# Kernel tuning notes

Measured on AMD Instinct MI355X. Metric: run time of the kernel, lower is better.

Reference implementation:

```python
import jax, jax.numpy as jnp
import numpy as np

N = 12288   # nodes
E = 393216  # edges (avg degree 32)
B = 16      # graphs in batch
F_IN = 15   # node feature dim
H = 32      # hidden_dim
EMB = 64    # embedding_dim
NC = 11     # num_classes
EDIM = 2    # edge feature dim
EPS = 1e-5  # BatchNorm eps


def _bn(x, gamma, beta):
    # training-mode BatchNorm1d: biased batch variance, matches torch normalization
    mu = jnp.mean(x, axis=0)
    var = jnp.var(x, axis=0)
    return gamma * (x - mu) * jax.lax.rsqrt(var + EPS) + beta


def setup_inputs() -> dict:
    key = jax.random.key(0)
    ks = jax.random.split(key, 16)
    def p(k, shape, s=0.05):
        return jax.random.normal(k, shape, dtype=jnp.float32) * s
    z = lambda *s: jnp.zeros(s, jnp.float32)
    o = lambda *s: jnp.ones(s, jnp.float32)
    return {
        "x": jax.random.normal(ks[0], (N, F_IN), dtype=jnp.float32),
        "edge_attr": jax.random.normal(ks[1], (E, EDIM), dtype=jnp.float32),
        "w_edge": p(ks[2], (EDIM, 1)), "b_edge": z(1),
        "w1": p(ks[3], (F_IN, H)), "b1": z(H), "g1": o(H), "be1": z(H),
        "w2": p(ks[4], (H, 2 * H)), "b2": z(2 * H), "g2": o(2 * H), "be2": z(2 * H),
        "w3": p(ks[5], (2 * H, EMB)), "b3": z(EMB), "g3": o(EMB), "be3": z(EMB),
        "wf1": p(ks[6], (EMB, 512)), "bf1": z(512), "gf1": o(512), "bef1": z(512),
        "wf2": p(ks[7], (512, 256)), "bf2": z(256), "gf2": o(256), "bef2": z(256),
        "wf3": p(ks[8], (256, NC)), "bf3": z(NC),
        "edge_index": jax.random.randint(ks[9], (2, E), 0, N, dtype=jnp.int64)
                      if jax.config.jax_enable_x64 else jax.random.randint(ks[9], (2, E), 0, N),
        "batch": jnp.sort(jax.random.randint(ks[10], (N,), 0, B)),
    }


def reference(x, edge_attr, w_edge, b_edge,
              w1, b1, g1, be1, w2, b2, g2, be2, w3, b3, g3, be3,
              wf1, bf1, gf1, bef1, wf2, bf2, gf2, bef2, wf3, bf3,
              edge_index, batch):
    # edge weights: sigmoid(Linear(edge_attr)) -> [E]
    ew = jax.nn.sigmoid(edge_attr @ w_edge + b_edge)[:, 0]
    # dense adjacency with self loops, accumulate duplicates (sparse_coo.to_dense)
    loop = jnp.arange(N)
    row = jnp.concatenate([edge_index[0], loop])
    col = jnp.concatenate([edge_index[1], loop])
    w_aug = jnp.concatenate([ew, jnp.ones((N,), ew.dtype)])
    adj = jnp.zeros((N, N), ew.dtype).at[row, col].add(w_aug)
    # symmetric degree normalization D^-1/2 A D^-1/2
    deg = adj.sum(axis=1)
    dis = jnp.where(deg > 0, jax.lax.rsqrt(jnp.where(deg > 0, deg, 1.0)), 0.0)
    support = dis[:, None] * adj * dis[None, :]
    # three GCN layers: support @ x @ W + b, BN, relu
    h = jax.nn.relu(_bn(support @ x @ w1 + b1, g1, be1))
    h = jax.nn.relu(_bn(support @ h @ w2 + b2, g2, be2))
    h = jax.nn.relu(_bn(support @ h @ w3 + b3, g3, be3))
    # global max pool per graph (empty graphs -> zeros)
    seg = jax.ops.segment_max(h, batch, num_segments=B)
    cnt = jax.ops.segment_sum(jnp.ones((N,), h.dtype), batch, num_segments=B)
    emb = jnp.where(cnt[:, None] > 0, seg, 0.0)
    # MLP head (dropout = identity at inference)
    o = jax.nn.relu(_bn(emb @ wf1 + bf1, gf1, bef1))
    o = jax.nn.relu(_bn(o @ wf2 + bf2, gf2, bef2))
    logits = o @ wf3 + bf3
    return jax.nn.log_softmax(logits, axis=1), emb
```

## Files before the change

kernel.cpp:

```cpp
#include <hip/hip_runtime.h>
#include <hip/hip_bf16.h>

#define NN   12288
#define EE   393216
#define EEPAD (EE + 8*NN)
#define BG   16
#define FIN  15
#define FH1  32
#define FH2  64
#define NCL  11
#define BNEPS 1e-5f
#define NBANK 32

typedef unsigned short u16;
typedef unsigned long long u64;
static inline int cdiv(long a, long b){ return (int)((a + b - 1) / b); }

__device__ __forceinline__ int getIdx(const void* p, long i, int is64){
  return is64 ? (int)((const long long*)p)[i] : ((const int*)p)[i];
}

__global__ void k_pre(u64* deg_cnt, float* csp1, float* csp2, float* csp3,
                      const void* ei, const void* batch, int* flags){
  int g = blockIdx.x*256 + threadIdx.x;
  if (g < NN) deg_cnt[g] = 0ull;
  if (g < NBANK*128){ csp1[g] = 0.f; csp2[g] = 0.f; csp3[g] = 0.f; }
  if (blockIdx.x == 0 && threadIdx.x < 64){
    const int* a = (const int*)ei;
    unsigned long long m0 = __ballot(a[2*threadIdx.x + 1] == 0);
    const int* b = (const int*)batch;
    int j = 96*threadIdx.x;
    unsigned long long m1 = __ballot(b[2*j + 1] == 0);
    if (threadIdx.x == 0){
      flags[0] = (m0 == ~0ull) ? 1 : 0;
      flags[1] = (m1 == ~0ull) ? 1 : 0;
    }
  }
}

__global__ void k_edge(const float* ea, const float* we, const float* bedg,
                       const void* ei, const int* flags, u64* deg_cnt, int* sslot){
  int e = blockIdx.x*256 + threadIdx.x;
  if (e >= EE) return;
  int is64 = flags[0];
  float z = ea[2*e]*we[0] + ea[2*e+1]*we[1] + bedg[0];
  float w = 1.0f/(1.0f + expf(-z));
  int r = getIdx(ei, e, is64);
  u64 add = (1ull << 32) | (u64)__float2uint_rn(w * 1048576.0f);
  u64 old = atomicAdd(&deg_cnt[r], add);
  sslot[e] = (int)(old >> 32);
}

__global__ void k_scanA(const u64* deg_cnt, int* rowptr, int* bsum){
  __shared__ int sbuf[256];
  int i = blockIdx.x*256 + threadIdx.x;
  int v = ((int)(deg_cnt[i] >> 32) + 7) & ~7;
  sbuf[threadIdx.x] = v;
  __syncthreads();
  for (int off = 1; off < 256; off <<= 1){
    int add = (threadIdx.x >= off) ? sbuf[threadIdx.x - off] : 0;
    __syncthreads();
    sbuf[threadIdx.x] += add;
    __syncthreads();
  }
  rowptr[i] = sbuf[threadIdx.x] - v;
  if (threadIdx.x == 255) bsum[blockIdx.x] = sbuf[255];
}

__global__ void k_scanB(const int* bsum, const u64* deg_cnt,
                        int* rowptr, float* dis, u64* csr_p){
  __shared__ int sbx[64];
  if (threadIdx.x < 64){
    int v = (threadIdx.x < 48) ? bsum[threadIdx.x] : 0;
    sbx[threadIdx.x] = v;
  }
  __syncthreads();
  for (int off = 1; off < 64; off <<= 1){
    int add = (threadIdx.x < 64 && threadIdx.x >= off) ? sbx[threadIdx.x - off] : 0;
    __syncthreads();
    if (threadIdx.x < 64) sbx[threadIdx.x] += add;
    __syncthreads();
  }
  __syncthreads();
  int off = (blockIdx.x == 0) ? 0 : sbx[blockIdx.x - 1];
  int i = blockIdx.x*256 + threadIdx.x;
  int rp = rowptr[i] + off;
  rowptr[i] = rp;
  u64 dc = deg_cnt[i];
  float deg = 1.0f + (float)(unsigned)(dc & 0xffffffffull) * (1.0f/1048576.0f);
  dis[i] = rsqrtf(deg);
  int n = (int)(dc >> 32), np = (n + 7) & ~7;
  for (int s = rp + n; s < rp + np; s++) csr_p[s] = 0ull;
}

__global__ void k_fill(const float* ea, const float* we, const float* bedg,
                       const void* ei, const int* flags, const float* dis,
                       const int* rowptr, const int* sslot, u64* csr_p){
  int e = blockIdx.x*256 + threadIdx.x;
  if (e >= EE) return;
  int is64 = flags[0];
  int r = getIdx(ei, e, is64);
  int c = getIdx(ei, (long)EE + e, is64);
  float z = ea[2*e]*we[0] + ea[2*e+1]*we[1] + bedg[0];
  float w = 1.0f/(1.0f + expf(-z));
  float wv = w * dis[c];
  int slot = rowptr[r] + sslot[e];
  csr_p[slot] = (u64)(unsigned)c | ((u64)__float_as_uint(wv) << 32);
}

template<int F, int FP, int FO, int APPLY_BN>
__global__ void __launch_bounds__(256) k_layer(
    const float* __restrict__ Hin, const float* __restrict__ csin,
    const float* __restrict__ g, const float* __restrict__ be,
    const float* __restrict__ W, const float* __restrict__ bias,
    const int* __restrict__ rowptr, const u64* __restrict__ deg_cnt,
    const u64* __restrict__ csr_p, const float* __restrict__ dis,
    float* __restrict__ Pout, float* __restrict__ csout){
  const int R = 256/FP;
  __shared__ float At[R][FP];
  __shared__ float lcs[FO], lcq[FO];
  if (threadIdx.x < FO){ lcs[threadIdx.x] = 0.f; lcq[threadIdx.x] = 0.f; }
  int f = threadIdx.x % FP, lr = threadIdx.x / FP;
  float sc = 1.f, sh = 0.f;
  if (APPLY_BN && f < F){
    float s = 0.f, q = 0.f;
    #pragma unroll
    for (int b = 0; b < NBANK; b++){ s += csin[b*128 + f]; q += csin[b*128 + 64 + f]; }
    float mu  = s*(1.0f/NN);
    float var = q*(1.0f/NN) - mu*mu;
    float rinv = rsqrtf(var + BNEPS);
    sc = g[f]*rinv; sh = be[f] - mu*sc;
  }
  int row = blockIdx.x*R + lr;
  if (f < F){
    float d = dis[row];
    float v0 = Hin[row*F + f];
    if (APPLY_BN) v0 = fmaxf(v0*sc + sh, 0.f);
    float acc = d * v0;
    int beg = rowptr[row];
    int n = (int)(deg_cnt[row] >> 32);
    int nch = (n + 7) >> 3;
    const uint4* pb = (const uint4*)(csr_p + beg);
    if (nch > 0){
      uint4 a0 = pb[0], a1 = pb[1], a2 = pb[2], a3 = pb[3];
      for (int ch = 0; ch < nch; ch++){
        uint4 b0, b1, b2, b3;
        bool more = (ch + 1 < nch);
        if (more){ b0 = pb[4*ch+4]; b1 = pb[4*ch+5]; b2 = pb[4*ch+6]; b3 = pb[4*ch+7]; }
        float h0 = Hin[(int)a0.x*F + f];
        float h1 = Hin[(int)a0.z*F + f];
        float h2 = Hin[(int)a1.x*F + f];
        float h3 = Hin[(int)a1.z*F + f];
        float h4 = Hin[(int)a2.x*F + f];
        float h5 = Hin[(int)a2.z*F + f];
        float h6 = Hin[(int)a3.x*F + f];
        float h7 = Hin[(int)a3.z*F + f];
        if (APPLY_BN){
          h0 = fmaxf(h0*sc + sh, 0.f); h1 = fmaxf(h1*sc + sh, 0.f);
          h2 = fmaxf(h2*sc + sh, 0.f); h3 = fmaxf(h3*sc + sh, 0.f);
          h4 = fmaxf(h4*sc + sh, 0.f); h5 = fmaxf(h5*sc + sh, 0.f);
          h6 = fmaxf(h6*sc + sh, 0.f); h7 = fmaxf(h7*sc + sh, 0.f);
        }
        acc += __uint_as_float(a0.y)*h0 + __uint_as_float(a0.w)*h1
             + __uint_as_float(a1.y)*h2 + __uint_as_float(a1.w)*h3
             + __uint_as_float(a2.y)*h4 + __uint_as_float(a2.w)*h5
             + __uint_as_float(a3.y)*h6 + __uint_as_float(a3.w)*h7;
        if (more){ a0 = b0; a1 = b1; a2 = b2; a3 = b3; }
      }
    }
    At[lr][f] = d * acc;
  }
  __syncthreads();
  const int fo = threadIdx.x % FO;
  float bb = bias[fo];
  for (int o = threadIdx.x; o < R*FO; o += 256){
    int l = o / FO;
    float s = bb;
    #pragma unroll
    for (int fi = 0; fi < F; fi++) s += At[l][fi] * W[fi*FO + fo];
    Pout[(blockIdx.x*R + l)*FO + fo] = s;
    atomicAdd(&lcs[fo], s);
    atomicAdd(&lcq[fo], s*s);
  }
  __syncthreads();
  if (threadIdx.x < FO){
    int bank = blockIdx.x & (NBANK-1);
    atomicAdd(&csout[bank*128 + threadIdx.x],      lcs[threadIdx.x]);
    atomicAdd(&csout[bank*128 + 64 + threadIdx.x], lcq[threadIdx.x]);
  }
}

__global__ void k_pool(const float* P3, const float* cs3, const float* g3,
                       const float* be3, const void* batch, const int* flags,
                       float* embf, float* out){
  int is64 = flags[1];
  int b = blockIdx.x;
  int lo = 0, hi = NN;
  while (lo < hi){ int m = (lo+hi)>>1; if (getIdx(batch, m, is64) < b) lo = m+1; else hi = m; }
  int start = lo;
  lo = start; hi = NN;
  while (lo < hi){ int m = (lo+hi)>>1; if (getIdx(batch, m, is64) < b+1) lo = m+1; else hi = m; }
  int end = lo;
  int f = threadIdx.x & 63, grp = threadIdx.x >> 6;
  float s = 0.f, q = 0.f;
  #pragma unroll
  for (int bk = 0; bk < NBANK; bk++){ s += cs3[bk*128 + f]; q += cs3[bk*128 + 64 + f]; }
  float mu  = s*(1.0f/NN);
  float var = q*(1.0f/NN) - mu*mu;
  float rinv = rsqrtf(var + BNEPS);
  float sc = g3[f]*rinv, sh = be3[f] - mu*sc;
  float m = 0.0f;
  for (int i = start + grp; i < end; i += 4)
    m = fmaxf(m, P3[(long)i*FH2 + f]*sc + sh);
  __shared__ float shm[4][64];
  shm[grp][f] = m;
  __syncthreads();
  if (grp == 0){
    float v = fmaxf(fmaxf(shm[0][f], shm[1][f]), fmaxf(shm[2][f], shm[3][f]));
    embf[b*64 + f] = v;
    out[BG*NCL + b*64 + f] = v;
  }
}

__global__ void __launch_bounds__(256) k_fcA(const float* embf, const float* wf1,
    const float* bf1, const float* gf1, const float* bef1, float* s1g){
  int c = blockIdx.x*4 + (threadIdx.x >> 6);
  int l = threadIdx.x & 63;
  float wcol = wf1[l*512 + c];
  float z[BG];
  #pragma unroll
  for (int r = 0; r < BG; r++){
    float v = embf[r*64 + l] * wcol;
    #pragma unroll
    for (int off = 32; off > 0; off >>= 1) v += __shfl_down(v, off);
    z[r] = v;
  }
  if (l == 0){
    float bb = bf1[c];
    float s = 0.f, q = 0.f;
    #pragma unroll
    for (int r = 0; r < BG; r++){ float zr = z[r] + bb; s += zr; q += zr*zr; }
    float mean = s*(1.f/BG), var = q*(1.f/BG) - mean*mean;
    float inv = rsqrtf(var + BNEPS);
    float gg = gf1[c], b2 = bef1[c];
    #pragma unroll
    for (int r = 0; r < BG; r++)
      s1g[r*512 + c] = fmaxf(gg*(z[r] + bb - mean)*inv + b2, 0.f);
  }
}

__global__ void __launch_bounds__(256) k_fcB(const float* s1g, const float* wf2,
    const float* bf2, const float* gf2, const float* bef2, float* s2g){
  int c = blockIdx.x*4 + (threadIdx.x >> 6);
  int l = threadIdx.x & 63;
  float wreg[8];
  #pragma unroll
  for (int j = 0; j < 8; j++) wreg[j] = wf2[(l + 64*j)*256 + c];
  float z[BG];
  #pragma unroll
  for (int r = 0; r < BG; r++){
    float v = 0.f;
    #pragma unroll
    for (int j = 0; j < 8; j++) v += s1g[r*512 + l + 64*j] * wreg[j];
    #pragma unroll
    for (int off = 32; off > 0; off >>= 1) v += __shfl_down(v, off);
    z[r] = v;
  }
  if (l == 0){
    float bb = bf2[c];
    float s = 0.f, q = 0.f;
    #pragma unroll
    for (int r = 0; r < BG; r++){ float zr = z[r] + bb; s += zr; q += zr*zr; }
    float mean = s*(1.f/BG), var = q*(1.f/BG) - mean*mean;
    float inv = rsqrtf(var + BNEPS);
    float gg = gf2[c], b2 = bef2[c];
    #pragma unroll
    for (int r = 0; r < BG; r++)
      s2g[r*256 + c] = fmaxf(gg*(z[r] + bb - mean)*inv + b2, 0.f);
  }
}

__global__ void k_fc3(const float* s2g, const float* wf3, const float* bf3, float* out){
  __shared__ float s2[BG*256];
  __shared__ float sl[BG*NCL];
  int t = threadIdx.x;
  for (int i = t; i < BG*256; i += 256) s2[i] = s2g[i];
  __syncthreads();
  if (t < BG*NCL){
    int r = t / NCL, c = t - r*NCL;
    float s = bf3[c];
    for (int k = 0; k < 256; k++) s += s2[r*256 + k]*wf3[k*NCL + c];
    sl[t] = s;
  }
  __syncthreads();
  if (t < BG){
    float m = -1e30f;
    for (int c = 0; c < NCL; c++) m = fmaxf(m, sl[t*NCL + c]);
    float s = 0.f;
    for (int c = 0; c < NCL; c++) s += expf(sl[t*NCL + c] - m);
    float lg = logf(s) + m;
    for (int c = 0; c < NCL; c++) out[t*NCL + c] = sl[t*NCL + c] - lg;
  }
}

extern "C" void kernel_launch(void* const* d_in, const int* in_sizes, int n_in,
                              void* d_out, int out_size, void* d_ws, size_t ws_size,
                              hipStream_t stream){
  const float* x    = (const float*)d_in[0];
  const float* ea   = (const float*)d_in[1];
  const float* we   = (const float*)d_in[2];
  const float* bedg = (const float*)d_in[3];
  const float* w1   = (const float*)d_in[4];  const float* b1  = (const float*)d_in[5];
  const float* g1   = (const float*)d_in[6];  const float* be1 = (const float*)d_in[7];
  const float* w2   = (const float*)d_in[8];  const float* b2  = (const float*)d_in[9];
  const float* g2   = (const float*)d_in[10]; const float* be2 = (const float*)d_in[11];
  const float* w3   = (const float*)d_in[12]; const float* b3  = (const float*)d_in[13];
  const float* g3   = (const float*)d_in[14]; const float* be3 = (const float*)d_in[15];
  const float* wf1  = (const float*)d_in[16]; const float* bf1 = (const float*)d_in[17];
  const float* gf1  = (const float*)d_in[18]; const float* bef1= (const float*)d_in[19];
  const float* wf2  = (const float*)d_in[20]; const float* bf2 = (const float*)d_in[21];
  const float* gf2  = (const float*)d_in[22]; const float* bef2= (const float*)d_in[23];
  const float* wf3  = (const float*)d_in[24]; const float* bf3 = (const float*)d_in[25];
  const void* ei    = d_in[26];
  const void* batch = d_in[27];
  float* out = (float*)d_out;

  u64* wq = (u64*)d_ws;
  u64* deg_cnt = wq; wq += NN;
  u64* csr_p   = wq; wq += EEPAD;
  float* ws = (float*)wq;
  float* dis   = ws; ws += NN;
  float* P1    = ws; ws += NN*FH1;
  float* P2    = ws; ws += NN*FH2;
  float* P3    = ws; ws += NN*FH2;
  float* csp1  = ws; ws += NBANK*128;
  float* csp2  = ws; ws += NBANK*128;
  float* csp3  = ws; ws += NBANK*128;
  float* embf  = ws; ws += BG*64;
  float* s1g   = ws; ws += BG*512;
  float* s2g   = ws; ws += BG*256;
  int* wi = (int*)ws;
  int* rowptr = wi; wi += NN;
  int* sslot  = wi; wi += EE;
  int* bsum   = wi; wi += 64;
  int* flags  = wi; wi += 2;

  k_pre<<<48, 256, 0, stream>>>(deg_cnt, csp1, csp2, csp3, ei, batch, flags);
  k_edge<<<cdiv(EE,256), 256, 0, stream>>>(ea, we, bedg, ei, flags, deg_cnt, sslot);
  k_scanA<<<48, 256, 0, stream>>>(deg_cnt, rowptr, bsum);
  k_scanB<<<48, 256, 0, stream>>>(bsum, deg_cnt, rowptr, dis, csr_p);
  k_fill<<<cdiv(EE,256), 256, 0, stream>>>(ea, we, bedg, ei, flags, dis, rowptr, sslot, csr_p);

  k_layer<FIN,16,FH1,0><<<NN/16, 256, 0, stream>>>(x, nullptr, nullptr, nullptr,
      w1, b1, rowptr, deg_cnt, csr_p, dis, P1, csp1);
  k_layer<FH1,32,FH2,1><<<NN/8, 256, 0, stream>>>(P1, csp1, g1, be1,
      w2, b2, rowptr, deg_cnt, csr_p, dis, P2, csp2);
  k_layer<FH2,64,FH2,1><<<NN/4, 256, 0, stream>>>(P2, csp2, g2, be2,
      w3, b3, rowptr, deg_cnt, csr_p, dis, P3, csp3);

  k_pool<<<BG, 256, 0, stream>>>(P3, csp3, g3, be3, batch, flags, embf, out);
  k_fcA<<<128, 256, 0, stream>>>(embf, wf1, bf1, gf1, bef1, s1g);
  k_fcB<<<64, 256, 0, stream>>>(s1g, wf2, bf2, gf2, bef2, s2g);
  k_fc3<<<1, 256, 0, stream>>>(s2g, wf3, bf3, out);
}
```

Measured before the change: 268.7 us.

## Replace scanned CSR with fixed-width ELL adjacency built in one edge pass

Builds the adjacency as a fixed 96-slot-per-row ELL buffer: the edge kernel writes each entry directly into its atomically claimed slot. This removes the two scan kernels, the separate fill pass and the rowptr/dis arrays. A new fix-up kernel applies the column degree normalization in place, and the layers compute the row scale from deg_cnt. The trade-off is a zero-fill plus a full pass over a ~9 MB padded buffer, and any row with more than 96 edges silently loses its extra edges.

```diff
diff --git a/kernel.cpp b/kernel.cpp
--- a/kernel.cpp
+++ b/kernel.cpp
@@ -3,7 +3,8 @@
 
 #define NN   12288
 #define EE   393216
-#define EEPAD (EE + 8*NN)
+#define WELL 96
+#define NELL (NN*WELL)
 #define BG   16
 #define FIN  15
 #define FH1  32
@@ -12,7 +13,6 @@
 #define BNEPS 1e-5f
 #define NBANK 32
 
-typedef unsigned short u16;
 typedef unsigned long long u64;
 static inline int cdiv(long a, long b){ return (int)((a + b - 1) / b); }
 
@@ -20,9 +20,14 @@
   return is64 ? (int)((const long long*)p)[i] : ((const int*)p)[i];
 }
 
-__global__ void k_pre(u64* deg_cnt, float* csp1, float* csp2, float* csp3,
-                      const void* ei, const void* batch, int* flags){
+__device__ __forceinline__ float degOf(u64 dc){
+  return 1.0f + (float)(unsigned)(dc & 0xffffffffull) * (1.0f/1048576.0f);
+}
+
+__global__ void k_pre(u64* deg_cnt, uint4* csr_q, float* csp1, float* csp2,
+                      float* csp3, const void* ei, const void* batch, int* flags){
   int g = blockIdx.x*256 + threadIdx.x;
+  if (g < NELL/2) csr_q[g] = make_uint4(0,0,0,0);
   if (g < NN) deg_cnt[g] = 0ull;
   if (g < NBANK*128){ csp1[g] = 0.f; csp2[g] = 0.f; csp3[g] = 0.f; }
   if (blockIdx.x == 0 && threadIdx.x < 64){
@@ -39,73 +44,30 @@
 }
 
 __global__ void k_edge(const float* ea, const float* we, const float* bedg,
-                       const void* ei, const int* flags, u64* deg_cnt, int* sslot){
+                       const void* ei, const int* flags, u64* deg_cnt, u64* csr_p){
   int e = blockIdx.x*256 + threadIdx.x;
   if (e >= EE) return;
   int is64 = flags[0];
   float z = ea[2*e]*we[0] + ea[2*e+1]*we[1] + bedg[0];
   float w = 1.0f/(1.0f + expf(-z));
   int r = getIdx(ei, e, is64);
+  int c = getIdx(ei, (long)EE + e, is64);
   u64 add = (1ull << 32) | (u64)__float2uint_rn(w * 1048576.0f);
   u64 old = atomicAdd(&deg_cnt[r], add);
-  sslot[e] = (int)(old >> 32);
-}
-
-__global__ void k_scanA(const u64* deg_cnt, int* rowptr, int* bsum){
-  __shared__ int sbuf[256];
-  int i = blockIdx.x*256 + threadIdx.x;
-  int v = ((int)(deg_cnt[i] >> 32) + 7) & ~7;
-  sbuf[threadIdx.x] = v;
-  __syncthreads();
-  for (int off = 1; off < 256; off <<= 1){
-    int add = (threadIdx.x >= off) ? sbuf[threadIdx.x - off] : 0;
-    __syncthreads();
-    sbuf[threadIdx.x] += add;
-    __syncthreads();
-  }
-  rowptr[i] = sbuf[threadIdx.x] - v;
-  if (threadIdx.x == 255) bsum[blockIdx.x] = sbuf[255];
-}
-
-__global__ void k_scanB(const int* bsum, const u64* deg_cnt,
-                        int* rowptr, float* dis, u64* csr_p){
-  __shared__ int sbx[64];
-  if (threadIdx.x < 64){
-    int v = (threadIdx.x < 48) ? bsum[threadIdx.x] : 0;
-    sbx[threadIdx.x] = v;
-  }
-  __syncthreads();
-  for (int off = 1; off < 64; off <<= 1){
-    int add = (threadIdx.x < 64 && threadIdx.x >= off) ? sbx[threadIdx.x - off] : 0;
-    __syncthreads();
-    if (threadIdx.x < 64) sbx[threadIdx.x] += add;
-    __syncthreads();
-  }
-  __syncthreads();
-  int off = (blockIdx.x == 0) ? 0 : sbx[blockIdx.x - 1];
-  int i = blockIdx.x*256 + threadIdx.x;
-  int rp = rowptr[i] + off;
-  rowptr[i] = rp;
-  u64 dc = deg_cnt[i];
-  float deg = 1.0f + (float)(unsigned)(dc & 0xffffffffull) * (1.0f/1048576.0f);
-  dis[i] = rsqrtf(deg);
-  int n = (int)(dc >> 32), np = (n + 7) & ~7;
-  for (int s = rp + n; s < rp + np; s++) csr_p[s] = 0ull;
-}
-
-__global__ void k_fill(const float* ea, const float* we, const float* bedg,
-                       const void* ei, const int* flags, const float* dis,
-                       const int* rowptr, const int* sslot, u64* csr_p){
-  int e = blockIdx.x*256 + threadIdx.x;
-  if (e >= EE) return;
-  int is64 = flags[0];
-  int r = getIdx(ei, e, is64);
-  int c = getIdx(ei, (long)EE + e, is64);
-  float z = ea[2*e]*we[0] + ea[2*e+1]*we[1] + bedg[0];
-  float w = 1.0f/(1.0f + expf(-z));
-  float wv = w * dis[c];
-  int slot = rowptr[r] + sslot[e];
-  csr_p[slot] = (u64)(unsigned)c | ((u64)__float_as_uint(wv) << 32);
+  int slot = (int)(old >> 32);
+  if (slot < WELL)
+    csr_p[r*WELL + slot] = (u64)(unsigned)c | ((u64)__float_as_uint(w) << 32);
+}
+
+__global__ void k_fix(u64* csr_p, const u64* deg_cnt){
+  int g = blockIdx.x*256 + threadIdx.x;
+  if (g >= NELL) return;
+  u64 v = csr_p[g];
+  unsigned wu = (unsigned)(v >> 32);
+  if (wu == 0u) return;
+  int c = (int)(unsigned)(v & 0xffffffffull);
+  float w = __uint_as_float(wu) * rsqrtf(degOf(deg_cnt[c]));
+  ((unsigned*)csr_p)[2*g + 1] = __float_as_uint(w);
 }
 
 template<int F, int FP, int FO, int APPLY_BN>
@@ -113,8 +75,7 @@
     const float* __restrict__ Hin, const float* __restrict__ csin,
     const float* __restrict__ g, const float* __restrict__ be,
     const float* __restrict__ W, const float* __restrict__ bias,
-    const int* __restrict__ rowptr, const u64* __restrict__ deg_cnt,
-    const u64* __restrict__ csr_p, const float* __restrict__ dis,
+    const u64* __restrict__ deg_cnt, const u64* __restrict__ csr_p,
     float* __restrict__ Pout, float* __restrict__ csout){
   const int R = 256/FP;
   __shared__ float At[R][FP];
@@ -133,14 +94,14 @@
   }
   int row = blockIdx.x*R + lr;
   if (f < F){
-    float d = dis[row];
+    u64 dc = deg_cnt[row];
+    float d = rsqrtf(degOf(dc));
+    int n = (int)(dc >> 32);
     float v0 = Hin[row*F + f];
     if (APPLY_BN) v0 = fmaxf(v0*sc + sh, 0.f);
     float acc = d * v0;
-    int beg = rowptr[row];
-    int n = (int)(deg_cnt[row] >> 32);
     int nch = (n + 7) >> 3;
-    const uint4* pb = (const uint4*)(csr_p + beg);
+    const uint4* pb = (const uint4*)(csr_p + row*WELL);
     if (nch > 0){
       uint4 a0 = pb[0], a1 = pb[1], a2 = pb[2], a3 = pb[3];
       for (int ch = 0; ch < nch; ch++){
@@ -327,9 +288,8 @@
 
   u64* wq = (u64*)d_ws;
   u64* deg_cnt = wq; wq += NN;
-  u64* csr_p   = wq; wq += EEPAD;
+  u64* csr_p   = wq; wq += NELL;
   float* ws = (float*)wq;
-  float* dis   = ws; ws += NN;
   float* P1    = ws; ws += NN*FH1;
   float* P2    = ws; ws += NN*FH2;
   float* P3    = ws; ws += NN*FH2;
@@ -339,24 +299,19 @@
   float* embf  = ws; ws += BG*64;
   float* s1g   = ws; ws += BG*512;
   float* s2g   = ws; ws += BG*256;
-  int* wi = (int*)ws;
-  int* rowptr = wi; wi += NN;
-  int* sslot  = wi; wi += EE;
-  int* bsum   = wi; wi += 64;
-  int* flags  = wi; wi += 2;
-
-  k_pre<<<48, 256, 0, stream>>>(deg_cnt, csp1, csp2, csp3, ei, batch, flags);
-  k_edge<<<cdiv(EE,256), 256, 0, stream>>>(ea, we, bedg, ei, flags, deg_cnt, sslot);
-  k_scanA<<<48, 256, 0, stream>>>(deg_cnt, rowptr, bsum);
-  k_scanB<<<48, 256, 0, stream>>>(bsum, deg_cnt, rowptr, dis, csr_p);
-  k_fill<<<cdiv(EE,256), 256, 0, stream>>>(ea, we, bedg, ei, flags, dis, rowptr, sslot, csr_p);
+  int* flags   = (int*)ws;
+
+  k_pre<<<cdiv(NELL/2,256), 256, 0, stream>>>(deg_cnt, (uint4*)csr_p,
+                                              csp1, csp2, csp3, ei, batch, flags);
+  k_edge<<<cdiv(EE,256), 256, 0, stream>>>(ea, we, bedg, ei, flags, deg_cnt, csr_p);
+  k_fix<<<cdiv(NELL,256), 256, 0, stream>>>(csr_p, deg_cnt);
 
   k_layer<FIN,16,FH1,0><<<NN/16, 256, 0, stream>>>(x, nullptr, nullptr, nullptr,
-      w1, b1, rowptr, deg_cnt, csr_p, dis, P1, csp1);
+      w1, b1, deg_cnt, csr_p, P1, csp1);
   k_layer<FH1,32,FH2,1><<<NN/8, 256, 0, stream>>>(P1, csp1, g1, be1,
-      w2, b2, rowptr, deg_cnt, csr_p, dis, P2, csp2);
+      w2, b2, deg_cnt, csr_p, P2, csp2);
   k_layer<FH2,64,FH2,1><<<NN/4, 256, 0, stream>>>(P2, csp2, g2, be2,
-      w3, b3, rowptr, deg_cnt, csr_p, dis, P3, csp3);
+      w3, b3, deg_cnt, csr_p, P3, csp3);
 
   k_pool<<<BG, 256, 0, stream>>>(P3, csp3, g3, be3, batch, flags, embf, out);
   k_fcA<<<128, 256, 0, stream>>>(embf, wf1, bf1, gf1, bef1, s1g);
```

New measurement: 265.7 us. No clear change (-1.1%).
